# Kernel tuning notes

Measured on AMD Instinct MI355X. Metric: run time of the kernel, lower is better.

## Reference

```python
import jax, jax.numpy as jnp
import numpy as np

N = 100000   # nodes
E = 1600000  # edges
DIN, DH, DOUT = 128, 64, 40
EPS = 1e-5


def setup_inputs() -> dict:
    key = jax.random.key(0)
    ks = jax.random.split(key, 16)
    glorot = lambda k, shp: jax.random.normal(k, shp, jnp.float32) / np.float32(np.sqrt(shp[0]))
    return {
        'x': jax.random.normal(ks[0], (N, DIN), jnp.float32),
        'edge_index': jax.random.randint(ks[1], (2, E), 0, N, jnp.int64),
        'W0': glorot(ks[2], (DIN, DH)), 'b0': jnp.zeros((DH,), jnp.float32),
        'W1': glorot(ks[3], (DH, DH)),  'b1': jnp.zeros((DH,), jnp.float32),
        'W2': glorot(ks[4], (DH, DH)),  'b2': jnp.zeros((DH,), jnp.float32),
        'ln0_g': jnp.ones((DH,), jnp.float32), 'ln0_b': jnp.zeros((DH,), jnp.float32),
        'ln1_g': jnp.ones((DH,), jnp.float32), 'ln1_b': jnp.zeros((DH,), jnp.float32),
        'mpW0': glorot(ks[5], (DH, DH)),  'mpb0': jnp.zeros((DH,), jnp.float32),
        'mpW1': glorot(ks[6], (DH, DOUT)), 'mpb1': jnp.zeros((DOUT,), jnp.float32),
    }


def _layernorm(h, g, b):
    mu = jnp.mean(h, axis=-1, keepdims=True)
    var = jnp.mean(jnp.square(h - mu), axis=-1, keepdims=True)
    return (h - mu) * jax.lax.rsqrt(var + EPS) * g + b


def _gcn_conv(x, src, dst, norm_e, self_w, W, b):
    # PyG GCNConv: h = x W; out = sum_{(s,d)} norm * h[s] scattered to d,
    # plus self-loop term, plus bias.  norm = d^{-1/2}[s] * d^{-1/2}[d] on A+I.
    h = x @ W                                        # [N, out]
    agg = jnp.zeros_like(h).at[dst].add(h[src] * norm_e[:, None])
    agg = agg + h * self_w[:, None]                  # self loops (i,i)
    return agg + b


def reference(x, edge_index, W0, b0, W1, b1, W2, b2,
              ln0_g, ln0_b, ln1_g, ln1_b, mpW0, mpb0, mpW1, mpb1):
    src, dst = edge_index[0], edge_index[1]
    # degree on A + I (count incoming edges at dst, +1 for self loop)
    deg = jnp.zeros((N,), jnp.float32).at[dst].add(1.0) + 1.0
    dinv = jax.lax.rsqrt(deg)
    norm_e = dinv[src] * dinv[dst]                   # per-edge weight [E]
    self_w = dinv * dinv                             # self-loop weight [N]

    h = x
    convs = [(W0, b0), (W1, b1), (W2, b2)]
    lns = [(ln0_g, ln0_b), (ln1_g, ln1_b)]
    for i, (W, b) in enumerate(convs):
        h = _gcn_conv(h, src, dst, norm_e, self_w, W, b)
        h = jax.nn.relu(h)
        # dropout: training=False -> identity
        if i != len(convs) - 1:
            g, bb = lns[i]
            h = _layernorm(h, g, bb)

    # post_mp: Linear -> Dropout(identity) -> Linear
    h = h @ mpW0 + mpb0
    return h @ mpW1 + mpb1
```

## Files before the change

kernel.cpp:

```cpp
#include <hip/hip_runtime.h>
#include <hip/hip_bf16.h>

#define NN 100000
#define EE 1600000
#define DOUT 40
#define LN_EPS 1e-5f
#define NBUCK 391
#define TILE 4096
#define TBLK 391
#define BCAP 8192

typedef __attribute__((ext_vector_type(8))) short short8;
typedef __attribute__((ext_vector_type(4))) float f32x4;

__device__ __forceinline__ float blo(unsigned u) { return __uint_as_float(u << 16); }
__device__ __forceinline__ float bhi(unsigned u) { return __uint_as_float(u & 0xffff0000u); }
__device__ __forceinline__ unsigned bpack(float lo, float hi) {
    unsigned a = __float_as_uint(lo);
    unsigned b = __float_as_uint(hi);
    a = (a + 0x7fffu + ((a >> 16) & 1u)) >> 16;
    b = (b + 0x7fffu + ((b >> 16) & 1u)) & 0xffff0000u;
    return (a & 0xffffu) | b;
}

__global__ __launch_bounds__(1024, 4) void bucket_k(
        const int* __restrict__ src, const int* __restrict__ dst,
        int* __restrict__ bucketCur, unsigned* __restrict__ bE,
        const float* __restrict__ W0, const float* __restrict__ W1,
        const float* __restrict__ W2,
        const float* __restrict__ mpW0, const float* __restrict__ mpb0,
        const float* __restrict__ mpW1, const float* __restrict__ mpb1,
        uint4* __restrict__ W0pk, uint4* __restrict__ W1pk,
        uint4* __restrict__ W2pk, uint4* __restrict__ Wfpk,
        float* __restrict__ bf) {
    __shared__ int cnt[8][NBUCK];
    __shared__ int basew[8][NBUCK];
    int tid = threadIdx.x;
    if (blockIdx.x == TBLK) {
        float* sWf = (float*)&basew[0][0];
        for (int i = tid; i < 64 * 48; i += 1024) {
            int k = i / 48, n = i % 48;
            float acc = 0.f;
            if (n < DOUT) {
                for (int j = 0; j < 64; ++j) acc = fmaf(mpW0[k * 64 + j], mpW1[j * DOUT + n], acc);
            }
            sWf[i] = acc;
        }
        for (int n = tid; n < 48; n += 1024) {
            float acc = 0.f;
            if (n < DOUT) {
                acc = mpb1[n];
                for (int j = 0; j < 64; ++j) acc = fmaf(mpb0[j], mpW1[j * DOUT + n], acc);
            }
            bf[n] = acc;
        }
        for (int i = tid; i < 1024; i += 1024) {
            int lane = i & 63, ct = i >> 6;
            int q = lane >> 4, ln = lane & 15;
            int c = ct >> 2, t = ct & 3;
            int row0 = c * 32 + q * 8, col = t * 16 + ln;
            uint4 u;
            u.x = bpack(W0[(row0 + 0) * 64 + col], W0[(row0 + 1) * 64 + col]);
            u.y = bpack(W0[(row0 + 2) * 64 + col], W0[(row0 + 3) * 64 + col]);
            u.z = bpack(W0[(row0 + 4) * 64 + col], W0[(row0 + 5) * 64 + col]);
            u.w = bpack(W0[(row0 + 6) * 64 + col], W0[(row0 + 7) * 64 + col]);
            W0pk[i] = u;
        }
        for (int i = tid; i < 512; i += 1024) {
            int lane = i & 63, ct = i >> 6;
            int q = lane >> 4, ln = lane & 15;
            int c = ct >> 2, t = ct & 3;
            int row0 = c * 32 + q * 8, col = t * 16 + ln;
            uint4 u;
            u.x = bpack(W1[(row0 + 0) * 64 + col], W1[(row0 + 1) * 64 + col]);
            u.y = bpack(W1[(row0 + 2) * 64 + col], W1[(row0 + 3) * 64 + col]);
            u.z = bpack(W1[(row0 + 4) * 64 + col], W1[(row0 + 5) * 64 + col]);
            u.w = bpack(W1[(row0 + 6) * 64 + col], W1[(row0 + 7) * 64 + col]);
            W1pk[i] = u;
            uint4 v;
            v.x = bpack(W2[(row0 + 0) * 64 + col], W2[(row0 + 1) * 64 + col]);
            v.y = bpack(W2[(row0 + 2) * 64 + col], W2[(row0 + 3) * 64 + col]);
            v.z = bpack(W2[(row0 + 4) * 64 + col], W2[(row0 + 5) * 64 + col]);
            v.w = bpack(W2[(row0 + 6) * 64 + col], W2[(row0 + 7) * 64 + col]);
            W2pk[i] = v;
        }
        __syncthreads();
        for (int i = tid; i < 384; i += 1024) {
            int lane = i & 63, ct = i >> 6;
            int q = lane >> 4, ln = lane & 15;
            int c = ct / 3, t = ct % 3;
            int row0 = c * 32 + q * 8, col = t * 16 + ln;
            uint4 u;
            u.x = bpack(sWf[(row0 + 0) * 48 + col], sWf[(row0 + 1) * 48 + col]);
            u.y = bpack(sWf[(row0 + 2) * 48 + col], sWf[(row0 + 3) * 48 + col]);
            u.z = bpack(sWf[(row0 + 4) * 48 + col], sWf[(row0 + 5) * 48 + col]);
            u.w = bpack(sWf[(row0 + 6) * 48 + col], sWf[(row0 + 7) * 48 + col]);
            Wfpk[i] = u;
        }
        return;
    }
    int hv = tid >> 7;
    for (int i = tid; i < 8 * NBUCK; i += 1024) ((int*)cnt)[i] = 0;
    __syncthreads();
    const int4* dst4 = (const int4*)dst;
    const int4* src4 = (const int4*)src;
    long i4 = (long)blockIdx.x * 1024 + tid;
    int4 dv = make_int4(-1, -1, -1, -1);
    int4 sv = make_int4(0, 0, 0, 0);
    if (i4 < EE / 4) { dv = dst4[i4]; sv = src4[i4]; }
    int d[4] = {dv.x, dv.y, dv.z, dv.w};
    int s[4] = {sv.x, sv.y, sv.z, sv.w};
#pragma unroll
    for (int i = 0; i < 4; ++i) {
        if (d[i] >= 0) atomicAdd(&cnt[hv][d[i] >> 8], 1);
    }
    __syncthreads();
    for (int b = tid; b < NBUCK; b += 1024) {
        int c[8];
        int tot = 0;
#pragma unroll
        for (int w = 0; w < 8; ++w) { c[w] = cnt[w][b]; tot += c[w]; }
        int base = tot ? atomicAdd(&bucketCur[b], tot) : 0;
        int run = b * BCAP + base;
#pragma unroll
        for (int w = 0; w < 8; ++w) { basew[w][b] = run; run += c[w]; cnt[w][b] = 0; }
    }
    __syncthreads();
#pragma unroll
    for (int i = 0; i < 4; ++i) {
        if (d[i] >= 0) {
            int b = d[i] >> 8;
            int pos = basew[hv][b] + atomicAdd(&cnt[hv][b], 1);
            bE[pos] = (unsigned)s[i] | ((unsigned)(d[i] & 255) << 24);
        }
    }
}

__global__ __launch_bounds__(1024, 4) void reorder2_k(const int* __restrict__ bucketCur,
                                                      const unsigned* __restrict__ bE,
                                                      int* __restrict__ csrSrc,
                                                      int* __restrict__ degI,
                                                      int* __restrict__ cursor,
                                                      float* __restrict__ dinv) {
    __shared__ int sScan[512];
    __shared__ int sHist[256];
    __shared__ int sPre[256];
    __shared__ int sStart[256];
    int tid = threadIdx.x;
    int b = blockIdx.x;
    if (tid < 512) sScan[tid] = (tid < NBUCK) ? bucketCur[tid] : 0;
    __syncthreads();
    for (int off = 1; off < 512; off <<= 1) {
        int t = (tid >= off && tid < 512) ? sScan[tid - off] : 0;
        __syncthreads();
        if (tid < 512) sScan[tid] += t;
        __syncthreads();
    }
    int bbase = (b == 0) ? 0 : sScan[b - 1];
    if (tid < 256) sHist[tid] = 0;
    __syncthreads();
    int start = b * BCAP;
    int ecnt = bucketCur[b];
    int nq = ecnt >> 2;
    const uint4* bE4 = (const uint4*)(bE + start);
    for (int i = tid; i < nq; i += 1024) {
        uint4 v = bE4[i];
        atomicAdd(&sHist[v.x >> 24], 1);
        atomicAdd(&sHist[v.y >> 24], 1);
        atomicAdd(&sHist[v.z >> 24], 1);
        atomicAdd(&sHist[v.w >> 24], 1);
    }
    for (int e = (nq << 2) + tid; e < ecnt; e += 1024) {
        atomicAdd(&sHist[bE[start + e] >> 24], 1);
    }
    __syncthreads();
    if (tid < 256) sPre[tid] = sHist[tid];
    __syncthreads();
    for (int off = 1; off < 256; off <<= 1) {
        int t = (tid >= off && tid < 256) ? sPre[tid - off] : 0;
        __syncthreads();
        if (tid < 256) sPre[tid] += t;
        __syncthreads();
    }
    if (tid < 256) {
        int h = sHist[tid];
        int excl = sPre[tid] - h;
        int st = bbase + excl;
        sStart[tid] = st;
        int nd = (b << 8) + tid;
        if (nd < NN) {
            degI[nd] = h;
            cursor[nd] = st;
            dinv[nd] = rsqrtf((float)h + 1.0f);
        }
    }
    __syncthreads();
    for (int i = tid; i < nq; i += 1024) {
        uint4 v = bE4[i];
        int p0 = atomicAdd(&sStart[v.x >> 24], 1);
        csrSrc[p0] = (int)(v.x & 0xFFFFFFu);
        int p1 = atomicAdd(&sStart[v.y >> 24], 1);
        csrSrc[p1] = (int)(v.y & 0xFFFFFFu);
        int p2 = atomicAdd(&sStart[v.z >> 24], 1);
        csrSrc[p2] = (int)(v.z & 0xFFFFFFu);
        int p3 = atomicAdd(&sStart[v.w >> 24], 1);
        csrSrc[p3] = (int)(v.w & 0xFFFFFFu);
    }
    for (int e = (nq << 2) + tid; e < ecnt; e += 1024) {
        unsigned v = bE[start + e];
        int pos = atomicAdd(&sStart[v >> 24], 1);
        csrSrc[pos] = (int)(v & 0xFFFFFFu);
    }
}

__global__ __launch_bounds__(256, 4) void gemm0(const float* __restrict__ X,
                                                const uint4* __restrict__ Wpk,
                                                const float* __restrict__ dinv,
                                                unsigned* __restrict__ H) {
    __shared__ float sD[64 * 65];
    int tid = threadIdx.x;
    int wv = tid >> 6, lane = tid & 63;
    int q = lane >> 4, ln = lane & 15;
    int base = blockIdx.x * 64;
    int node = base + wv * 16 + ln;
    bool ok = node < NN;
    short8 afrag[4];
#pragma unroll
    for (int c = 0; c < 4; ++c) {
        float4 f0 = make_float4(0.f, 0.f, 0.f, 0.f);
        float4 f1 = make_float4(0.f, 0.f, 0.f, 0.f);
        if (ok) {
            const float4* xp = (const float4*)(X + (long)node * 128 + c * 32 + q * 8);
            f0 = xp[0];
            f1 = xp[1];
        }
        uint4 u;
        u.x = bpack(f0.x, f0.y);
        u.y = bpack(f0.z, f0.w);
        u.z = bpack(f1.x, f1.y);
        u.w = bpack(f1.z, f1.w);
        afrag[c] = __builtin_bit_cast(short8, u);
    }
#pragma unroll
    for (int t = 0; t < 4; ++t) {
        f32x4 acc = {0.f, 0.f, 0.f, 0.f};
#pragma unroll
        for (int c = 0; c < 4; ++c) {
            short8 bfrag = __builtin_bit_cast(short8, Wpk[(c * 4 + t) * 64 + lane]);
            acc = __builtin_amdgcn_mfma_f32_16x16x32_bf16(afrag[c], bfrag, acc, 0, 0, 0);
        }
#pragma unroll
        for (int r = 0; r < 4; ++r)
            sD[(wv * 16 + q * 4 + r) * 65 + t * 16 + ln] = acc[r];
    }
    __syncthreads();
    for (int i = tid; i < 64 * 32; i += 256) {
        int row = i >> 5, c2 = i & 31;
        int nd = base + row;
        if (nd < NN) {
            float di = dinv[nd];
            float lo = sD[row * 65 + c2 * 2] * di;
            float hi = sD[row * 65 + c2 * 2 + 1] * di;
            H[nd * 32 + c2] = bpack(lo, hi);
        }
    }
}

template <int DOLN, int FINAL>
__global__ __launch_bounds__(1024, 8) void aggf_k(
        const int* __restrict__ cursor, const int* __restrict__ degI,
        const int* __restrict__ csrSrc, const float* __restrict__ dinv,
        const uint2* __restrict__ H2, const float4* __restrict__ bias4,
        const float4* __restrict__ g4, const float4* __restrict__ beta4,
        const uint4* __restrict__ Wpk, const float* __restrict__ bfv,
        unsigned* __restrict__ Hout, float* __restrict__ outF) {
    __shared__ __align__(16) unsigned sH[16][36];
    __shared__ float sD[16 * 65];
    int tid = threadIdx.x;
    int wv = tid >> 6, lane = tid & 63;
    int g = lane >> 4;
    unsigned f = (unsigned)(lane & 15);
    unsigned node = (unsigned)(blockIdx.x * 16 + wv);
    int start = cursor[node];
    int deg = degI[node];
    int myIdx = 0;
    if (lane < deg) myIdx = csrSrc[(unsigned)(start + lane)];
    uint2 qs = H2[node * 16u + f];
    float di = dinv[node];
    float4 bb = bias4[f];
    float ax = 0.f, ay = 0.f, az = 0.f, aw = 0.f;
    float bx = 0.f, by = 0.f, bz = 0.f, bw = 0.f;
    uint2 qa[4];
#pragma unroll
    for (int r = 0; r < 4; ++r) {
        int e = r * 4 + g;
        unsigned s = (unsigned)__shfl(myIdx, e);
        qa[r] = make_uint2(0u, 0u);
        if (e < deg) qa[r] = H2[s * 16u + f];
    }
    if (deg <= 16) {
#pragma unroll
        for (int r = 0; r < 4; r += 2) {
            ax += blo(qa[r].x);     ay += bhi(qa[r].x);
            az += blo(qa[r].y);     aw += bhi(qa[r].y);
            bx += blo(qa[r + 1].x); by += bhi(qa[r + 1].x);
            bz += blo(qa[r + 1].y); bw += bhi(qa[r + 1].y);
        }
    } else {
        uint2 qb[4];
#pragma unroll
        for (int r = 0; r < 4; ++r) {
            int e = 16 + r * 4 + g;
            unsigned s = (unsigned)__shfl(myIdx, e);
            qb[r] = make_uint2(0u, 0u);
            if (e < deg) qb[r] = H2[s * 16u + f];
        }
#pragma unroll
        for (int r = 0; r < 4; r += 2) {
            ax += blo(qa[r].x);     ay += bhi(qa[r].x);
            az += blo(qa[r].y);     aw += bhi(qa[r].y);
            bx += blo(qa[r + 1].x); by += bhi(qa[r + 1].x);
            bz += blo(qa[r + 1].y); bw += bhi(qa[r + 1].y);
        }
#pragma unroll
        for (int r = 0; r < 4; r += 2) {
            ax += blo(qb[r].x);     ay += bhi(qb[r].x);
            az += blo(qb[r].y);     aw += bhi(qb[r].y);
            bx += blo(qb[r + 1].x); by += bhi(qb[r + 1].x);
            bz += blo(qb[r + 1].y); bw += bhi(qb[r + 1].y);
        }
        if (deg > 32) {
            int R2 = (deg + 3) >> 2;
            if (R2 > 16) R2 = 16;
            for (int r = 8; r < R2; ++r) {
                int e = r * 4 + g;
                unsigned s = (unsigned)__shfl(myIdx, e);
                uint2 qq = make_uint2(0u, 0u);
                if (e < deg) qq = H2[s * 16u + f];
                ax += blo(qq.x); ay += bhi(qq.x); az += blo(qq.y); aw += bhi(qq.y);
            }
            for (int ee = 64 + g; ee < deg; ee += 4) {
                uint2 qq = H2[(unsigned)csrSrc[(unsigned)(start + ee)] * 16u + f];
                ax += blo(qq.x); ay += bhi(qq.x); az += blo(qq.y); aw += bhi(qq.y);
            }
        }
    }
    ax += bx; ay += by; az += bz; aw += bw;
    ax += __shfl_xor(ax, 16); ay += __shfl_xor(ay, 16);
    az += __shfl_xor(az, 16); aw += __shfl_xor(aw, 16);
    ax += __shfl_xor(ax, 32); ay += __shfl_xor(ay, 32);
    az += __shfl_xor(az, 32); aw += __shfl_xor(aw, 32);
    float vx = fmaxf((ax + blo(qs.x)) * di + bb.x, 0.f);
    float vy = fmaxf((ay + bhi(qs.x)) * di + bb.y, 0.f);
    float vz = fmaxf((az + blo(qs.y)) * di + bb.z, 0.f);
    float vw = fmaxf((aw + bhi(qs.y)) * di + bb.w, 0.f);
    if (DOLN) {
        float s = vx + vy + vz + vw;
        s += __shfl_xor(s, 1); s += __shfl_xor(s, 2);
        s += __shfl_xor(s, 4); s += __shfl_xor(s, 8);
        float mu = s * (1.f / 64.f);
        vx -= mu; vy -= mu; vz -= mu; vw -= mu;
        float vs = vx * vx + vy * vy + vz * vz + vw * vw;
        vs += __shfl_xor(vs, 1); vs += __shfl_xor(vs, 2);
        vs += __shfl_xor(vs, 4); vs += __shfl_xor(vs, 8);
        float inv = rsqrtf(vs * (1.f / 64.f) + LN_EPS);
        float4 gg = g4[f];
        float4 tt = beta4[f];
        vx = vx * inv * gg.x + tt.x;
        vy = vy * inv * gg.y + tt.y;
        vz = vz * inv * gg.z + tt.z;
        vw = vw * inv * gg.w + tt.w;
    }
    if (g == 0) {
        sH[wv][2 * f] = bpack(vx, vy);
        sH[wv][2 * f + 1] = bpack(vz, vw);
    }
    __syncthreads();
    constexpr int NT = FINAL ? 3 : 4;
    if (wv < NT) {
        int q = lane >> 4, ln = lane & 15;
        short8 a0 = __builtin_bit_cast(short8, ((const uint4*)sH[ln])[q]);
        short8 a1 = __builtin_bit_cast(short8, ((const uint4*)sH[ln])[4 + q]);
        f32x4 acc = {0.f, 0.f, 0.f, 0.f};
        acc = __builtin_amdgcn_mfma_f32_16x16x32_bf16(
            a0, __builtin_bit_cast(short8, Wpk[(0 * NT + wv) * 64 + lane]), acc, 0, 0, 0);
        acc = __builtin_amdgcn_mfma_f32_16x16x32_bf16(
            a1, __builtin_bit_cast(short8, Wpk[(1 * NT + wv) * 64 + lane]), acc, 0, 0, 0);
#pragma unroll
        for (int r = 0; r < 4; ++r)
            sD[(q * 4 + r) * 65 + wv * 16 + ln] = acc[r];
    }
    __syncthreads();
    if (FINAL) {
        for (int i = tid; i < 16 * DOUT; i += 1024) {
            int row = i / DOUT, col = i % DOUT;
            unsigned nd = (unsigned)(blockIdx.x * 16 + row);
            outF[nd * (unsigned)DOUT + col] = sD[row * 65 + col] + bfv[col];
        }
    } else {
        for (int i = tid; i < 16 * 32; i += 1024) {
            int row = i >> 5, c2 = i & 31;
            unsigned nd = (unsigned)(blockIdx.x * 16 + row);
            float dn = dinv[nd];
            Hout[nd * 32u + c2] = bpack(sD[row * 65 + c2 * 2] * dn,
                                        sD[row * 65 + c2 * 2 + 1] * dn);
        }
    }
}

extern "C" void kernel_launch(void* const* d_in, const int* in_sizes, int n_in,
                              void* d_out, int out_size, void* d_ws, size_t ws_size,
                              hipStream_t stream) {
    const float* x    = (const float*)d_in[0];
    const int*   ei   = (const int*)d_in[1];
    const int*   srcI = ei;
    const int*   dstI = ei + EE;
    const float* W0   = (const float*)d_in[2];
    const float* b0   = (const float*)d_in[3];
    const float* W1   = (const float*)d_in[4];
    const float* b1   = (const float*)d_in[5];
    const float* W2   = (const float*)d_in[6];
    const float* b2   = (const float*)d_in[7];
    const float* ln0g = (const float*)d_in[8];
    const float* ln0b = (const float*)d_in[9];
    const float* ln1g = (const float*)d_in[10];
    const float* ln1b = (const float*)d_in[11];
    const float* mpW0 = (const float*)d_in[12];
    const float* mpb0 = (const float*)d_in[13];
    const float* mpW1 = (const float*)d_in[14];
    const float* mpb1 = (const float*)d_in[15];
    float* out = (float*)d_out;

    char* ws = (char*)d_ws;
    float*    dinv      = (float*)   (ws + 0);
    int*      degI      = (int*)     (ws + 512l * 1024);
    int*      cursor    = (int*)     (ws + 1024l * 1024);
    int*      bucketCur = (int*)     (ws + 1600l * 1024);
    uint4*    W0pk      = (uint4*)   (ws + 1792l * 1024);
    uint4*    W1pk      = (uint4*)   (ws + 1824l * 1024);
    uint4*    W2pk      = (uint4*)   (ws + 1856l * 1024);
    uint4*    Wfpk      = (uint4*)   (ws + 1888l * 1024);
    float*    bfv       = (float*)   (ws + 1920l * 1024);
    unsigned* bE        = (unsigned*)(ws + 2048l * 1024);
    int*      csrSrc    = (int*)     (ws + 15l * 1024 * 1024);
    unsigned* bufA      = (unsigned*)(ws + 22l * 1024 * 1024);
    unsigned* bufB      = (unsigned*)(ws + 36l * 1024 * 1024);

    const int aggBlocks  = NN / 16;
    const int gemmBlocks = (NN + 63) / 64;

    hipMemsetAsync(bucketCur, 0, NBUCK * sizeof(int), stream);
    bucket_k<<<TBLK + 1, 1024, 0, stream>>>(srcI, dstI, bucketCur, bE,
                                            W0, W1, W2, mpW0, mpb0, mpW1, mpb1,
                                            W0pk, W1pk, W2pk, Wfpk, bfv);
    reorder2_k<<<NBUCK, 1024, 0, stream>>>(bucketCur, bE, csrSrc, degI, cursor, dinv);

    gemm0<<<gemmBlocks, 256, 0, stream>>>(x, W0pk, dinv, bufA);
    aggf_k<1, 0><<<aggBlocks, 1024, 0, stream>>>(cursor, degI, csrSrc, dinv,
                                                 (const uint2*)bufA, (const float4*)b0,
                                                 (const float4*)ln0g, (const float4*)ln0b,
                                                 W1pk, bfv, bufB, out);
    aggf_k<1, 0><<<aggBlocks, 1024, 0, stream>>>(cursor, degI, csrSrc, dinv,
                                                 (const uint2*)bufB, (const float4*)b1,
                                                 (const float4*)ln1g, (const float4*)ln1b,
                                                 W2pk, bfv, bufA, out);
    aggf_k<0, 1><<<aggBlocks, 1024, 0, stream>>>(cursor, degI, csrSrc, dinv,
                                                 (const uint2*)bufA, (const float4*)b2,
                                                 (const float4*)ln0g, (const float4*)ln0b,
                                                 Wfpk, bfv, bufB, out);
}
```

Baseline: 307.9 us.

## Make aggregation waves independent: per-wave MFMA via shuffles, no shared memory

Each wave now does the dense projection for its own node. It builds the MFMA A operand with lane shuffles (the other 15 rows are copies) and writes outputs directly, which removes the shared-memory staging and both block-wide barriers. Blocks shrink from 1024 to 256 threads with four nodes per block. This drops synchronisation stalls and lets waves stall independently on irregular neighbour gathers. The cost is redundant MFMA work, since each wave runs all NT tiles for a single useful row, plus extra shuffles and less coalesced narrow stores.

```diff
diff --git a/kernel.cpp b/kernel.cpp
--- a/kernel.cpp
+++ b/kernel.cpp
@@ -267,20 +267,18 @@
 }
 
 template <int DOLN, int FINAL>
-__global__ __launch_bounds__(1024, 8) void aggf_k(
+__global__ __launch_bounds__(256, 4) void aggf_k(
         const int* __restrict__ cursor, const int* __restrict__ degI,
         const int* __restrict__ csrSrc, const float* __restrict__ dinv,
         const uint2* __restrict__ H2, const float4* __restrict__ bias4,
         const float4* __restrict__ g4, const float4* __restrict__ beta4,
         const uint4* __restrict__ Wpk, const float* __restrict__ bfv,
         unsigned* __restrict__ Hout, float* __restrict__ outF) {
-    __shared__ __align__(16) unsigned sH[16][36];
-    __shared__ float sD[16 * 65];
     int tid = threadIdx.x;
-    int wv = tid >> 6, lane = tid & 63;
+    int w = tid >> 6, lane = tid & 63;
     int g = lane >> 4;
     unsigned f = (unsigned)(lane & 15);
-    unsigned node = (unsigned)(blockIdx.x * 16 + wv);
+    unsigned node = (unsigned)(blockIdx.x * 4 + w);
     int start = cursor[node];
     int deg = degI[node];
     int myIdx = 0;
@@ -371,39 +369,36 @@
         vz = vz * inv * gg.z + tt.z;
         vw = vw * inv * gg.w + tt.w;
     }
-    if (g == 0) {
-        sH[wv][2 * f] = bpack(vx, vy);
-        sH[wv][2 * f + 1] = bpack(vz, vw);
-    }
-    __syncthreads();
+    int q2 = (lane >> 4) * 2;
+    float c0x = __shfl(vx, q2),     c0y = __shfl(vy, q2);
+    float c0z = __shfl(vz, q2),     c0w = __shfl(vw, q2);
+    float c1x = __shfl(vx, q2 + 1), c1y = __shfl(vy, q2 + 1);
+    float c1z = __shfl(vz, q2 + 1), c1w = __shfl(vw, q2 + 1);
+    float c2x = __shfl(vx, q2 + 8), c2y = __shfl(vy, q2 + 8);
+    float c2z = __shfl(vz, q2 + 8), c2w = __shfl(vw, q2 + 8);
+    float c3x = __shfl(vx, q2 + 9), c3y = __shfl(vy, q2 + 9);
+    float c3z = __shfl(vz, q2 + 9), c3w = __shfl(vw, q2 + 9);
+    uint4 ua0 = make_uint4(bpack(c0x, c0y), bpack(c0z, c0w), bpack(c1x, c1y), bpack(c1z, c1w));
+    uint4 ua1 = make_uint4(bpack(c2x, c2y), bpack(c2z, c2w), bpack(c3x, c3y), bpack(c3z, c3w));
+    short8 a0 = __builtin_bit_cast(short8, ua0);
+    short8 a1 = __builtin_bit_cast(short8, ua1);
     constexpr int NT = FINAL ? 3 : 4;
-    if (wv < NT) {
-        int q = lane >> 4, ln = lane & 15;
-        short8 a0 = __builtin_bit_cast(short8, ((const uint4*)sH[ln])[q]);
-        short8 a1 = __builtin_bit_cast(short8, ((const uint4*)sH[ln])[4 + q]);
+#pragma unroll
+    for (int t = 0; t < NT; ++t) {
         f32x4 acc = {0.f, 0.f, 0.f, 0.f};
         acc = __builtin_amdgcn_mfma_f32_16x16x32_bf16(
-            a0, __builtin_bit_cast(short8, Wpk[(0 * NT + wv) * 64 + lane]), acc, 0, 0, 0);
+            a0, __builtin_bit_cast(short8, Wpk[(0 * NT + t) * 64 + lane]), acc, 0, 0, 0);
         acc = __builtin_amdgcn_mfma_f32_16x16x32_bf16(
-            a1, __builtin_bit_cast(short8, Wpk[(1 * NT + wv) * 64 + lane]), acc, 0, 0, 0);
-#pragma unroll
-        for (int r = 0; r < 4; ++r)
-            sD[(q * 4 + r) * 65 + wv * 16 + ln] = acc[r];
-    }
-    __syncthreads();
-    if (FINAL) {
-        for (int i = tid; i < 16 * DOUT; i += 1024) {
-            int row = i / DOUT, col = i % DOUT;
-            unsigned nd = (unsigned)(blockIdx.x * 16 + row);
-            outF[nd * (unsigned)DOUT + col] = sD[row * 65 + col] + bfv[col];
-        }
-    } else {
-        for (int i = tid; i < 16 * 32; i += 1024) {
-            int row = i >> 5, c2 = i & 31;
-            unsigned nd = (unsigned)(blockIdx.x * 16 + row);
-            float dn = dinv[nd];
-            Hout[nd * 32u + c2] = bpack(sD[row * 65 + c2 * 2] * dn,
-                                        sD[row * 65 + c2 * 2 + 1] * dn);
+            a1, __builtin_bit_cast(short8, Wpk[(1 * NT + t) * 64 + lane]), acc, 0, 0, 0);
+        if (FINAL) {
+            int col = t * 16 + lane;
+            if (lane < 16 && col < DOUT) outF[node * (unsigned)DOUT + col] = acc[0] + bfv[col];
+        } else {
+            float vv = acc[0] * di;
+            float lo = __shfl(vv, lane & ~1);
+            float hi = __shfl(vv, (lane & ~1) | 1);
+            if (lane < 16 && !(lane & 1))
+                Hout[node * 32u + t * 8 + (lane >> 1)] = bpack(lo, hi);
         }
     }
 }
@@ -446,7 +441,7 @@
     unsigned* bufA      = (unsigned*)(ws + 22l * 1024 * 1024);
     unsigned* bufB      = (unsigned*)(ws + 36l * 1024 * 1024);
 
-    const int aggBlocks  = NN / 16;
+    const int aggBlocks  = NN / 4;
     const int gemmBlocks = (NN + 63) / 64;
 
     hipMemsetAsync(bucketCur, 0, NBUCK * sizeof(int), stream);
@@ -456,16 +451,16 @@
     reorder2_k<<<NBUCK, 1024, 0, stream>>>(bucketCur, bE, csrSrc, degI, cursor, dinv);
 
     gemm0<<<gemmBlocks, 256, 0, stream>>>(x, W0pk, dinv, bufA);
-    aggf_k<1, 0><<<aggBlocks, 1024, 0, stream>>>(cursor, degI, csrSrc, dinv,
-                                                 (const uint2*)bufA, (const float4*)b0,
-                                                 (const float4*)ln0g, (const float4*)ln0b,
-                                                 W1pk, bfv, bufB, out);
-    aggf_k<1, 0><<<aggBlocks, 1024, 0, stream>>>(cursor, degI, csrSrc, dinv,
-                                                 (const uint2*)bufB, (const float4*)b1,
-                                                 (const float4*)ln1g, (const float4*)ln1b,
-                                                 W2pk, bfv, bufA, out);
-    aggf_k<0, 1><<<aggBlocks, 1024, 0, stream>>>(cursor, degI, csrSrc, dinv,
-                                                 (const uint2*)bufA, (const float4*)b2,
-                                                 (const float4*)ln0g, (const float4*)ln0b,
-                                                 Wfpk, bfv, bufB, out);
-}
+    aggf_k<1, 0><<<aggBlocks, 256, 0, stream>>>(cursor, degI, csrSrc, dinv,
+                                                (const uint2*)bufA, (const float4*)b0,
+                                                (const float4*)ln0g, (const float4*)ln0b,
+                                                W1pk, bfv, bufB, out);
+    aggf_k<1, 0><<<aggBlocks, 256, 0, stream>>>(cursor, degI, csrSrc, dinv,
+                                                (const uint2*)bufB, (const float4*)b1,
+                                                (const float4*)ln1g, (const float4*)ln1b,
+                                                W2pk, bfv, bufA, out);
+    aggf_k<0, 1><<<aggBlocks, 256, 0, stream>>>(cursor, degI, csrSrc, dinv,
+                                                (const uint2*)bufA, (const float4*)b2,
+                                                (const float4*)ln0g, (const float4*)ln0b,
+                                                Wfpk, bfv, bufB, out);
+}
```

Measured after the change: 346.0 us. +12.4%, slower.
